# Performance work log

Measured on AMD Instinct MI355X. Metric: run time of the kernel, lower is better.

## Reference

```python
import jax, jax.numpy as jnp
import numpy as np

N_KERNELS = 11

def _kernel_mus(n):
    l = [1.0]
    bs = 2.0 / (n - 1)
    l.append(1 - bs / 2)
    for i in range(1, n - 1):
        l.append(l[i] - bs)
    return l

def _kernel_sigmas(n):
    bs = 2.0 / (n - 1)
    return [0.001] + [0.5 * bs] * (n - 1)

MU = jnp.asarray(_kernel_mus(N_KERNELS), jnp.float32)      # [K]
SIGMA = jnp.asarray(_kernel_sigmas(N_KERNELS), jnp.float32)  # [K]


def setup_inputs() -> dict:
    key = jax.random.key(0)
    ks = jax.random.split(key, 10)
    V, E, C = 50000, 300, 128
    B, Q, D = 128, 30, 200
    inp = {
        'query_tokens': jax.random.randint(ks[0], (B, Q), 0, V),
        'document_tokens': jax.random.randint(ks[1], (B, D), 0, V),
        'embedding': jax.random.normal(ks[2], (V, E), jnp.float32) * 0.1,
        'conv_w1': jax.random.normal(ks[3], (C, E, 1), jnp.float32) * 0.05,
        'conv_w2': jax.random.normal(ks[4], (C, E, 2), jnp.float32) * 0.05,
        'conv_w3': jax.random.normal(ks[5], (C, E, 3), jnp.float32) * 0.05,
        'conv_b1': jax.random.normal(ks[6], (C,), jnp.float32) * 0.01,
        'conv_b2': jax.random.normal(ks[7], (C,), jnp.float32) * 0.01,
        'conv_b3': jax.random.normal(ks[8], (C,), jnp.float32) * 0.01,
        'dense_w': jax.random.uniform(ks[9], (1, N_KERNELS * 9), jnp.float32, -0.014, 0.014),
    }
    return inp


def _conv_ngram(x_ble, w, b):
    # x_ble: [B, L, E]; w: [C, E, k]; pad (0, k-1) on the length dim -> same length out
    x = x_ble.transpose(0, 2, 1)  # [B, E, L]
    y = jax.lax.conv_general_dilated(
        x, w, window_strides=(1,), padding=[(0, w.shape[2] - 1)],
        dimension_numbers=('NCH', 'OIH', 'NCH'))
    return jax.nn.relu(y + b[None, :, None]).transpose(0, 2, 1)  # [B, L, C]


def _kernel_pool(q, d, qd_mask, q_mask):
    # q: [B,Q,C], d: [B,D,C]; cosine sim -> Gaussian RBF soft-binning -> masked log-sum pooling
    qn = q / (jnp.linalg.norm(q, axis=-1, keepdims=True) + 1e-13)
    dn = d / (jnp.linalg.norm(d, axis=-1, keepdims=True) + 1e-13)
    cos = jnp.einsum('bqc,bdc->bqd', qn, dn) * qd_mask           # [B,Q,D]
    diff = cos[..., None] - MU                                    # [B,Q,D,K]
    kern = jnp.exp(-(diff * diff) / (2.0 * SIGMA * SIGMA)) * qd_mask[..., None]
    per_kernel_query = jnp.sum(kern, axis=2)                      # [B,Q,K]
    logk = jnp.log(jnp.clip(per_kernel_query, 1e-10)) * 0.01
    return jnp.sum(logk * q_mask[..., None], axis=1)              # [B,K]


def reference(query_tokens, document_tokens, embedding,
              conv_w1, conv_w2, conv_w3, conv_b1, conv_b2, conv_b3, dense_w):
    q_mask = (query_tokens > 0).astype(jnp.float32)               # [B,Q]
    d_mask = (document_tokens > 0).astype(jnp.float32)            # [B,D]
    qd_mask = q_mask[:, :, None] * d_mask[:, None, :]             # [B,Q,D]

    q_emb = embedding[query_tokens]                               # [B,Q,E]
    d_emb = embedding[document_tokens]                            # [B,D,E]

    convs = [(conv_w1, conv_b1), (conv_w2, conv_b2), (conv_w3, conv_b3)]
    q_grams = [_conv_ngram(q_emb, w, b) for w, b in convs]
    d_grams = [_conv_ngram(d_emb, w, b) for w, b in convs]

    feats = jnp.concatenate(
        [_kernel_pool(q, d, qd_mask, q_mask) for q in q_grams for d in d_grams],
        axis=1)                                                   # [B, K*9]
    return (feats @ dense_w.T)[:, 0]                              # [B]
```

## Files before the change

### kernel.cpp

```cpp
#include <hip/hip_runtime.h>
#include <hip/hip_bf16.h>
#include <math.h>

#define B_   128
#define Qn   30
#define Dn   200
#define En   300

typedef __attribute__((ext_vector_type(8))) short short8;
typedef __attribute__((ext_vector_type(4))) float floatx4;
typedef unsigned int u32;
typedef unsigned short u16;

typedef const __attribute__((address_space(1))) unsigned int* gas_ptr;
typedef __attribute__((address_space(3))) unsigned int* las_ptr;

static __device__ __forceinline__ void gld_lds16(const void* g, void* l) {
    __builtin_amdgcn_global_load_lds((gas_ptr)g, (las_ptr)l, 16, 0, 0);
}

static __device__ __forceinline__ u16 f2b(float x) {
    union { float f; u32 u; } v; v.f = x;
    u32 r = v.u + 0x7FFFu + ((v.u >> 16) & 1u);
    return (u16)(r >> 16);
}
static __device__ __forceinline__ float bits2f(u32 u) {
    union { u32 u2; float f; } v; v.u2 = u; return v.f;
}

__global__ void prep_gather_kernel(
    const int* __restrict__ qtok, const int* __restrict__ dtok,
    const float* __restrict__ emb,
    const float* __restrict__ w1, const float* __restrict__ w2, const float* __restrict__ w3,
    u16* __restrict__ Ag, u16* __restrict__ Wt2)
{
    const int tid = threadIdx.x;
    if (blockIdx.x < 16) {
        const int b = blockIdx.y, c = blockIdx.x;
        __shared__ int toks[16];
        if (tid < 16) {
            int pos = c*16 + tid;
            int tok = -1;
            if (pos < Dn) tok = dtok[b*Dn + pos];
            else if (pos >= 208 && pos < 238) tok = qtok[b*Qn + (pos - 208)];
            toks[tid] = tok;
        }
        __syncthreads();
        #pragma unroll
        for (int i = 0; i < 5; ++i) {
            int f = tid + i*256;
            int r = f / 80, c4 = f - r*80;
            int t = toks[r];
            u16 o0=0,o1=0,o2=0,o3=0;
            if (t >= 0 && c4 < 75) {
                float4 v = *(const float4*)(emb + t*En + c4*4);
                o0=f2b(v.x); o1=f2b(v.y); o2=f2b(v.z); o3=f2b(v.w);
            }
            u16* p = Ag + ((b*256 + c*16 + r)*320 + c4*4);
            p[0]=o0; p[1]=o1; p[2]=o2; p[3]=o3;
        }
        if (b == 127 && c == 15 && tid < 160) {
            u16* p = Ag + (32768*320) + tid*4;
            p[0]=0; p[1]=0; p[2]=0; p[3]=0;
        }
    } else {
        int p = ((blockIdx.x - 16)*128 + blockIdx.y)*256 + tid;
        if (p >= 245760) return;
        int g, ntap, o;
        if (p < 40960)       { g=0; ntap=1; o=p; }
        else if (p < 122880) { g=1; ntap=2; o=p-40960; }
        else                 { g=2; ntap=3; o=p-122880; }
        int ks = o / (ntap*4096);
        int r  = o - ks*(ntap*4096);
        int j  = r / 4096;
        int r2 = r & 4095;
        int nt = r2 >> 9;
        int r3 = r2 & 511;
        int q4 = r3 >> 7;
        int c16 = (r3 >> 3) & 15;
        int k8 = r3 & 7;
        int ch = nt*16 + c16;
        int e  = ks*32 + q4*8 + k8;
        float v = 0.f;
        if (e < En) {
            if (g == 0)      v = w1[ch*En + e];
            else if (g == 1) v = w2[(ch*En + e)*2 + j];
            else             v = w3[(ch*En + e)*3 + j];
        }
        Wt2[p] = f2b(v);
    }
}

template<int NTAP>
static __device__ __forceinline__ void conv_body64(
    int tile, int gram,
    const u16* __restrict__ Ag, const u16* __restrict__ Wt2g,
    const float* __restrict__ bp,
    u16* __restrict__ qg, u16* __restrict__ dg,
    float* __restrict__ invnq, float* __restrict__ invnd, char* smem)
{
    char* As  = smem;
    char* Bs0 = smem + 43296;
    char* Bs1 = smem + 43296 + NTAP*8192;

    const int tid = threadIdx.x;
    const int wv = tid >> 6, lane = tid & 63;
    const int l15 = lane & 15, qd4 = lane >> 4;
    const int mh = wv >> 1, nh = wv & 1;

    {
        const char* src = (const char*)Wt2g + lane*16;
        #pragma unroll
        for (int i = 0; i < NTAP*2; ++i) {
            int chunk = wv*NTAP*2 + i;
            gld_lds16(src + chunk*1024, Bs0 + chunk*1024);
        }
    }
    {
        const char* base = (const char*)Ag + (size_t)tile*64*640;
        #pragma unroll
        for (int i = 0; i < 11; ++i) {
            int idx = tid + i*256;
            if (idx < 2640) {
                int r = idx / 40, c = idx - r*40;
                uint4 v = *(const uint4*)(base + r*640 + c*16);
                *(uint4*)(As + r*656 + c*16) = v;
            }
        }
    }

    float bias[4];
    #pragma unroll
    for (int nt = 0; nt < 4; ++nt) bias[nt] = bp[nh*64 + nt*16 + l15];

    floatx4 acc[2][4];
    #pragma unroll
    for (int mt = 0; mt < 2; ++mt)
        #pragma unroll
        for (int nt = 0; nt < 4; ++nt)
            acc[mt][nt] = (floatx4){0.f,0.f,0.f,0.f};

    __syncthreads();

    for (int ks = 0; ks < 10; ++ks) {
        char* Bcur = (ks & 1) ? Bs1 : Bs0;
        char* Bnxt = (ks & 1) ? Bs0 : Bs1;
        if (ks < 9) {
            const char* src = (const char*)Wt2g + (ks+1)*NTAP*8192 + lane*16;
            #pragma unroll
            for (int i = 0; i < NTAP*2; ++i) {
                int chunk = wv*NTAP*2 + i;
                gld_lds16(src + chunk*1024, Bnxt + chunk*1024);
            }
        }
        short8 af[2][NTAP];
        #pragma unroll
        for (int mt = 0; mt < 2; ++mt)
            #pragma unroll
            for (int j = 0; j < NTAP; ++j)
                af[mt][j] = *(const short8*)(As + (mh*32 + mt*16 + l15 + j)*656 + ks*64 + qd4*16);
        #pragma unroll
        for (int j = 0; j < NTAP; ++j) {
            short8 bfj[4];
            #pragma unroll
            for (int nt = 0; nt < 4; ++nt)
                bfj[nt] = *(const short8*)(Bcur + (j*8 + nh*4 + nt)*1024 + lane*16);
            #pragma unroll
            for (int mt = 0; mt < 2; ++mt)
                #pragma unroll
                for (int nt = 0; nt < 4; ++nt)
                    acc[mt][nt] = __builtin_amdgcn_mfma_f32_16x16x32_bf16(
                        af[mt][j], bfj[nt], acc[mt][nt], 0, 0, 0);
        }
        __syncthreads();
    }

    u16* Gs = (u16*)As;
    #pragma unroll
    for (int mt = 0; mt < 2; ++mt)
        #pragma unroll
        for (int nt = 0; nt < 4; ++nt) {
            int ch = nh*64 + nt*16 + l15;
            #pragma unroll
            for (int i = 0; i < 4; ++i) {
                int row = mh*32 + mt*16 + qd4*4 + i;
                Gs[row*136 + ch] = f2b(fmaxf(acc[mt][nt][i] + bias[nt], 0.f));
            }
        }
    __syncthreads();

    if (tid < 64) {
        const char* rp = (const char*)Gs + tid*272;
        float ssum = 0.f;
        #pragma unroll
        for (int t16 = 0; t16 < 16; ++t16) {
            uint4 u = *(const uint4*)(rp + t16*16);
            float x;
            x = bits2f(u.x << 16); ssum += x*x;  x = bits2f(u.x & 0xffff0000u); ssum += x*x;
            x = bits2f(u.y << 16); ssum += x*x;  x = bits2f(u.y & 0xffff0000u); ssum += x*x;
            x = bits2f(u.z << 16); ssum += x*x;  x = bits2f(u.z & 0xffff0000u); ssum += x*x;
            x = bits2f(u.w << 16); ssum += x*x;  x = bits2f(u.w & 0xffff0000u); ssum += x*x;
        }
        float inv = 1.f / (sqrtf(ssum) + 1e-13f);
        int gR = tile*64 + tid;
        int b = gR >> 8, pos = gR & 255;
        if (pos < 208)      invnd[(gram*B_ + b)*208 + pos] = inv;
        else if (pos < 238) invnq[(gram*B_ + b)*32 + (pos - 208)] = inv;
    }
    #pragma unroll
    for (int i = 0; i < 4; ++i) {
        int idx = tid + i*256;
        int r = idx >> 4, c16 = idx & 15;
        uint4 v = *(const uint4*)((const char*)Gs + r*272 + c16*16);
        int gR = tile*64 + r;
        int b = gR >> 8, pos = gR & 255;
        if (pos < 208)      *(uint4*)(dg + ((gram*B_ + b)*208 + pos)*128 + c16*8) = v;
        else if (pos < 238) *(uint4*)(qg + ((gram*B_ + b)*32 + (pos - 208))*128 + c16*8) = v;
    }
}

static __device__ __forceinline__ void conv_body32(
    int tile,
    const u16* __restrict__ Ag, const u16* __restrict__ Wt2g,
    const float* __restrict__ bp,
    u16* __restrict__ qg, u16* __restrict__ dg,
    float* __restrict__ invnq, float* __restrict__ invnd, char* smem)
{
    char* As  = smem;
    char* Bs0 = smem + 22304;
    char* Bs1 = smem + 46880;

    const int tid = threadIdx.x;
    const int wv = tid >> 6, lane = tid & 63;
    const int l15 = lane & 15, qd4 = lane >> 4;

    {
        const char* src = (const char*)Wt2g + lane*16;
        #pragma unroll
        for (int i = 0; i < 6; ++i) {
            int chunk = wv*6 + i;
            gld_lds16(src + chunk*1024, Bs0 + chunk*1024);
        }
    }
    {
        const char* base = (const char*)Ag + (size_t)tile*32*640;
        #pragma unroll
        for (int i = 0; i < 6; ++i) {
            int idx = tid + i*256;
            if (idx < 1360) {
                int r = idx / 40, c = idx - r*40;
                uint4 v = *(const uint4*)(base + r*640 + c*16);
                *(uint4*)(As + r*656 + c*16) = v;
            }
        }
    }

    float bias[2];
    #pragma unroll
    for (int nt = 0; nt < 2; ++nt) bias[nt] = bp[wv*32 + nt*16 + l15];

    floatx4 acc[2][2];
    #pragma unroll
    for (int mt = 0; mt < 2; ++mt)
        #pragma unroll
        for (int nt = 0; nt < 2; ++nt)
            acc[mt][nt] = (floatx4){0.f,0.f,0.f,0.f};

    __syncthreads();

    for (int ks = 0; ks < 10; ++ks) {
        char* Bcur = (ks & 1) ? Bs1 : Bs0;
        char* Bnxt = (ks & 1) ? Bs0 : Bs1;
        if (ks < 9) {
            const char* src = (const char*)Wt2g + (ks+1)*24576 + lane*16;
            #pragma unroll
            for (int i = 0; i < 6; ++i) {
                int chunk = wv*6 + i;
                gld_lds16(src + chunk*1024, Bnxt + chunk*1024);
            }
        }
        short8 af[2][3];
        #pragma unroll
        for (int mt = 0; mt < 2; ++mt)
            #pragma unroll
            for (int j = 0; j < 3; ++j)
                af[mt][j] = *(const short8*)(As + (mt*16 + l15 + j)*656 + ks*64 + qd4*16);
        #pragma unroll
        for (int j = 0; j < 3; ++j) {
            short8 bfj[2];
            #pragma unroll
            for (int nt = 0; nt < 2; ++nt)
                bfj[nt] = *(const short8*)(Bcur + (j*8 + wv*2 + nt)*1024 + lane*16);
            #pragma unroll
            for (int mt = 0; mt < 2; ++mt)
                #pragma unroll
                for (int nt = 0; nt < 2; ++nt)
                    acc[mt][nt] = __builtin_amdgcn_mfma_f32_16x16x32_bf16(
                        af[mt][j], bfj[nt], acc[mt][nt], 0, 0, 0);
        }
        __syncthreads();
    }

    u16* Gs = (u16*)As;
    #pragma unroll
    for (int mt = 0; mt < 2; ++mt)
        #pragma unroll
        for (int nt = 0; nt < 2; ++nt) {
            int ch = wv*32 + nt*16 + l15;
            #pragma unroll
            for (int i = 0; i < 4; ++i) {
                int row = mt*16 + qd4*4 + i;
                Gs[row*136 + ch] = f2b(fmaxf(acc[mt][nt][i] + bias[nt], 0.f));
            }
        }
    __syncthreads();

    if (tid < 32) {
        const char* rp = (const char*)Gs + tid*272;
        float ssum = 0.f;
        #pragma unroll
        for (int t16 = 0; t16 < 16; ++t16) {
            uint4 u = *(const uint4*)(rp + t16*16);
            float x;
            x = bits2f(u.x << 16); ssum += x*x;  x = bits2f(u.x & 0xffff0000u); ssum += x*x;
            x = bits2f(u.y << 16); ssum += x*x;  x = bits2f(u.y & 0xffff0000u); ssum += x*x;
            x = bits2f(u.z << 16); ssum += x*x;  x = bits2f(u.z & 0xffff0000u); ssum += x*x;
            x = bits2f(u.w << 16); ssum += x*x;  x = bits2f(u.w & 0xffff0000u); ssum += x*x;
        }
        float inv = 1.f / (sqrtf(ssum) + 1e-13f);
        int gR = tile*32 + tid;
        int b = gR >> 8, pos = gR & 255;
        if (pos < 208)      invnd[(2*B_ + b)*208 + pos] = inv;
        else if (pos < 238) invnq[(2*B_ + b)*32 + (pos - 208)] = inv;
    }
    #pragma unroll
    for (int i = 0; i < 2; ++i) {
        int idx = tid + i*256;
        int r = idx >> 4, c16 = idx & 15;
        uint4 v = *(const uint4*)((const char*)Gs + r*272 + c16*16);
        int gR = tile*32 + r;
        int b = gR >> 8, pos = gR & 255;
        if (pos < 208)      *(uint4*)(dg + ((2*B_ + b)*208 + pos)*128 + c16*8) = v;
        else if (pos < 238) *(uint4*)(qg + ((2*B_ + b)*32 + (pos - 208))*128 + c16*8) = v;
    }
}

__global__ __launch_bounds__(256, 2) void conv_kernel(
    const u16* __restrict__ Ag, const u16* __restrict__ Wt2,
    const float* __restrict__ b1, const float* __restrict__ b2, const float* __restrict__ b3,
    u16* __restrict__ qg, u16* __restrict__ dg,
    float* __restrict__ invnq, float* __restrict__ invnd)
{
    extern __shared__ char smem[];
    int bx = blockIdx.x;
    if (bx < 512)
        conv_body64<1>(bx,      0, Ag, Wt2,        b1, qg, dg, invnq, invnd, smem);
    else if (bx < 1024)
        conv_body64<2>(bx-512,  1, Ag, Wt2+40960,  b2, qg, dg, invnq, invnd, smem);
    else
        conv_body32(bx-1024,       Ag, Wt2+122880, b3, qg, dg, invnq, invnd, smem);
}

__global__ __launch_bounds__(256, 2) void pool_kernel(
    const u16* __restrict__ qg, const u16* __restrict__ dg,
    const float* __restrict__ invnq, const float* __restrict__ invnd,
    const int* __restrict__ qtok, const int* __restrict__ dtok,
    float* __restrict__ feats)
{
    __shared__ __align__(16) u16 dsb[208*136];
    __shared__ float pk[96*12];
    __shared__ float invqA[96];
    __shared__ float qmA[96];
    __shared__ __align__(16) float invd[208];

    const int tid = threadIdx.x;
    const int b = blockIdx.y, dj = blockIdx.x;
    const int wv = tid >> 6, lane = tid & 63;
    const int l15 = lane & 15, qd4 = lane >> 4;

    for (int idx = tid; idx < 208*16; idx += 256) {
        int r = idx >> 4, ch = idx & 15;
        uint4 v = make_uint4(0u,0u,0u,0u);
        if (r < Dn) v = *(const uint4*)(dg + ((dj*B_ + b)*208 + r)*128 + ch*8);
        *(uint4*)((char*)dsb + r*272 + ch*16) = v;
    }
    if (tid < 208) {
        float v = invnd[(dj*B_ + b)*208 + tid];
        bool ok = (tid < Dn) && (dtok[b*Dn + tid] > 0);
        invd[tid] = ok ? v : (-fabsf(v) - 1.0f);
    }
    if (tid < 96) {
        int qi = tid >> 5, qr = tid & 31;
        float v = invnq[(qi*B_ + b)*32 + qr];
        bool ok = (qr < Qn) && (qtok[b*Qn + qr] > 0);
        invqA[tid] = ok ? v : 0.f;
        qmA[tid] = ok ? 1.f : 0.f;
    }
    for (int i = tid; i < 96*12; i += 256) pk[i] = 0.f;
    __syncthreads();

    const float CkR[9] = {8886110.5f, 162754.79f, 2980.958f, 54.598150f, 1.0f,
                          0.018315639f, 3.3546263e-4f, 6.1442124e-6f, 1.1253517e-7f};

    for (int qi = 0; qi < 3; ++qi) {
        short8 qf[2][4];
        float vq[2];
        #pragma unroll
        for (int qt = 0; qt < 2; ++qt) {
            vq[qt] = invqA[qi*32 + qt*16 + l15];
            #pragma unroll
            for (int ks = 0; ks < 4; ++ks)
                qf[qt][ks] = *(const short8*)(qg + ((qi*B_ + b)*32 + qt*16 + l15)*128 + ks*32 + qd4*8);
        }
        float pkl[2][11];
        #pragma unroll
        for (int qt = 0; qt < 2; ++qt)
            #pragma unroll
            for (int k = 0; k < 11; ++k) pkl[qt][k] = 0.f;

        for (int t = wv; t < 13; t += 4) {
            short8 af[4];
            #pragma unroll
            for (int ks = 0; ks < 4; ++ks)
                af[ks] = *(const short8*)((const char*)dsb + (t*16 + l15)*272 + ks*64 + qd4*16);
            floatx4 acc[2];
            acc[0] = (floatx4){0.f,0.f,0.f,0.f};
            acc[1] = (floatx4){0.f,0.f,0.f,0.f};
            #pragma unroll
            for (int ks = 0; ks < 4; ++ks)
                #pragma unroll
                for (int qt = 0; qt < 2; ++qt)
                    acc[qt] = __builtin_amdgcn_mfma_f32_16x16x32_bf16(af[ks], qf[qt][ks], acc[qt], 0, 0, 0);
            floatx4 iv4 = *(const floatx4*)(invd + t*16 + qd4*4);
            #pragma unroll
            for (int qt = 0; qt < 2; ++qt)
                #pragma unroll
                for (int i = 0; i < 4; ++i) {
                    float cs = acc[qt][i] * vq[qt] * iv4[i];
                    cs = (cs > 0.f) ? cs : 2.0f;
                    float t0 = cs - 1.0f;
                    float u  = cs - 0.9f;
                    float s0 = __expf(-500000.f * t0 * t0);
                    float e  = __expf(-50.f * u * u);
                    float rr = __expf(-20.f * cs);
                    pkl[qt][0] += s0;
                    pkl[qt][1] += e;
                    #pragma unroll
                    for (int kk = 0; kk < 9; ++kk) {
                        e = e * rr * CkR[kk];
                        pkl[qt][2 + kk] += e;
                    }
                }
        }
        #pragma unroll
        for (int qt = 0; qt < 2; ++qt)
            #pragma unroll
            for (int k = 0; k < 11; ++k) {
                float v = pkl[qt][k];
                v += __shfl_xor(v, 16);
                v += __shfl_xor(v, 32);
                if (qd4 == 0) atomicAdd(&pk[(qi*32 + qt*16 + l15)*12 + k], v);
            }
    }
    __syncthreads();

    if (tid < 33) {
        int qi = tid / 11, k = tid - qi*11;
        float s = 0.f;
        for (int q = 0; q < Qn; ++q)
            s += qmA[qi*32 + q] * 0.01f * __logf(fmaxf(pk[(qi*32 + q)*12 + k], 1e-10f));
        feats[(b*9 + qi*3 + dj)*11 + k] = s;
    }
}

__global__ void final_kernel(const float* __restrict__ feats,
                             const float* __restrict__ dw,
                             float* __restrict__ out) {
    int b = threadIdx.x;
    if (b < B_) {
        float s = 0.f;
        for (int f = 0; f < 99; ++f) s += feats[b*99 + f] * dw[f];
        out[b] = s;
    }
}

extern "C" void kernel_launch(void* const* d_in, const int* in_sizes, int n_in,
                              void* d_out, int out_size, void* d_ws, size_t ws_size,
                              hipStream_t stream) {
    const int*   qtok = (const int*)d_in[0];
    const int*   dtok = (const int*)d_in[1];
    const float* emb  = (const float*)d_in[2];
    const float* w1   = (const float*)d_in[3];
    const float* w2   = (const float*)d_in[4];
    const float* w3   = (const float*)d_in[5];
    const float* b1   = (const float*)d_in[6];
    const float* b2   = (const float*)d_in[7];
    const float* b3   = (const float*)d_in[8];
    const float* dw   = (const float*)d_in[9];
    float* out = (float*)d_out;

    char* w = (char*)d_ws;
    u16*   Wt2   = (u16*)w;
    u16*   Ag    = (u16*)(w + 491520);
    u16*   qg    = (u16*)(w + 21464320);
    u16*   dgm   = (u16*)(w + 24610048);
    float* invq_ = (float*)(w + 45057280);
    float* invd_ = (float*)(w + 45106432);
    float* feats = (float*)(w + 45425920);

    prep_gather_kernel<<<dim3(24, B_), 256, 0, stream>>>(
        qtok, dtok, emb, w1, w2, w3, Ag, Wt2);

    const int conv_lds = 76064;
    hipFuncSetAttribute(reinterpret_cast<const void*>(conv_kernel),
                        hipFuncAttributeMaxDynamicSharedMemorySize, conv_lds);
    conv_kernel<<<dim3(2048), 256, conv_lds, stream>>>(
        Ag, Wt2, b1, b2, b3, qg, dgm, invq_, invd_);

    pool_kernel<<<dim3(3, B_), 256, 0, stream>>>(qg, dgm, invq_, invd_, qtok, dtok, feats);

    final_kernel<<<1, 128, 0, stream>>>(feats, dw, out);
}
```

Baseline: 183.1 us.

## Fuse embedding gather into conv and compute all three n-grams per tile

The embedding gather and bf16 conversion move from the prep kernel into the conv kernel, so the intermediate bf16 gathered matrix is no longer written to and re-read from global memory. Each 64-row tile now computes all three n-gram convolutions at once with 512 threads, sharing the A tile in LDS and interleaving the weights for all grams per k-step. The launch drops from 2048 blocks to 512. The cost is a much larger LDS footprint (about 141KB per block), which likely limits residency to one block per CU, and the embedding gather latency now sits inside the conv kernel.

New measurement: 173.6 us. 5.2% less time.

```diff
diff --git a/kernel.cpp b/kernel.cpp
--- a/kernel.cpp
+++ b/kernel.cpp
@@ -28,117 +28,109 @@
     union { u32 u2; float f; } v; v.u2 = u; return v.f;
 }
 
-__global__ void prep_gather_kernel(
+__global__ void prep_kernel(
+    const float* __restrict__ w1, const float* __restrict__ w2, const float* __restrict__ w3,
+    u16* __restrict__ Wt3)
+{
+    int p = (blockIdx.x*128 + blockIdx.y)*256 + threadIdx.x;
+    if (p >= 245760) return;
+    int ks = p / 24576;
+    int r  = p - ks*24576;
+    int g, rr;
+    if (r < 4096)        { g = 0; rr = r;         }
+    else if (r < 12288)  { g = 1; rr = r - 4096;  }
+    else                 { g = 2; rr = r - 12288; }
+    int j  = rr >> 12;
+    int r2 = rr & 4095;
+    int nt  = r2 >> 9;
+    int q4  = (r2 >> 7) & 3;
+    int c16 = (r2 >> 3) & 15;
+    int k8  = r2 & 7;
+    int ch = nt*16 + c16;
+    int e  = ks*32 + q4*8 + k8;
+    float v = 0.f;
+    if (e < En) {
+        if (g == 0)      v = w1[ch*En + e];
+        else if (g == 1) v = w2[(ch*En + e)*2 + j];
+        else             v = w3[(ch*En + e)*3 + j];
+    }
+    Wt3[p] = f2b(v);
+}
+
+__global__ __launch_bounds__(512, 2) void conv_kernel(
     const int* __restrict__ qtok, const int* __restrict__ dtok,
     const float* __restrict__ emb,
-    const float* __restrict__ w1, const float* __restrict__ w2, const float* __restrict__ w3,
-    u16* __restrict__ Ag, u16* __restrict__ Wt2)
+    const u16* __restrict__ Wt3,
+    const float* __restrict__ b1, const float* __restrict__ b2, const float* __restrict__ b3,
+    u16* __restrict__ qg, u16* __restrict__ dg,
+    float* __restrict__ invnq, float* __restrict__ invnd)
 {
+    extern __shared__ char smem[];
+    char* As  = smem;
+    char* Bs0 = smem + 43296;
+    char* Bs1 = smem + 92448;
+    int*  toks = (int*)(smem + 141600);
+
+    const int tile = blockIdx.x;
     const int tid = threadIdx.x;
-    if (blockIdx.x < 16) {
-        const int b = blockIdx.y, c = blockIdx.x;
-        __shared__ int toks[16];
-        if (tid < 16) {
-            int pos = c*16 + tid;
-            int tok = -1;
-            if (pos < Dn) tok = dtok[b*Dn + pos];
-            else if (pos >= 208 && pos < 238) tok = qtok[b*Qn + (pos - 208)];
-            toks[tid] = tok;
-        }
-        __syncthreads();
-        #pragma unroll
-        for (int i = 0; i < 5; ++i) {
-            int f = tid + i*256;
-            int r = f / 80, c4 = f - r*80;
+    const int wv = tid >> 6, lane = tid & 63;
+    const int l15 = lane & 15, qd4 = lane >> 4;
+    const int mh = wv >> 2, nh = wv & 3;
+    const int gR0 = tile*64;
+
+    if (tid < 66) {
+        int gr = gR0 + tid;
+        int t = -1;
+        if (gr < 32768) {
+            int b = gr >> 8, pos = gr & 255;
+            if (pos < Dn) t = dtok[b*Dn + pos];
+            else if (pos >= 208 && pos < 238) t = qtok[b*Qn + (pos - 208)];
+        }
+        toks[tid] = t;
+    }
+    __syncthreads();
+
+    {
+        const char* src = (const char*)Wt3 + lane*16;
+        #pragma unroll
+        for (int i = 0; i < 6; ++i) {
+            int chunk = wv*6 + i;
+            gld_lds16(src + chunk*1024, Bs0 + chunk*1024);
+        }
+    }
+    #pragma unroll
+    for (int i = 0; i < 11; ++i) {
+        int idx = tid + i*512;
+        if (idx < 5280) {
+            int r = idx / 80, c4 = idx - r*80;
             int t = toks[r];
             u16 o0=0,o1=0,o2=0,o3=0;
             if (t >= 0 && c4 < 75) {
                 float4 v = *(const float4*)(emb + t*En + c4*4);
                 o0=f2b(v.x); o1=f2b(v.y); o2=f2b(v.z); o3=f2b(v.w);
             }
-            u16* p = Ag + ((b*256 + c*16 + r)*320 + c4*4);
-            p[0]=o0; p[1]=o1; p[2]=o2; p[3]=o3;
-        }
-        if (b == 127 && c == 15 && tid < 160) {
-            u16* p = Ag + (32768*320) + tid*4;
-            p[0]=0; p[1]=0; p[2]=0; p[3]=0;
-        }
-    } else {
-        int p = ((blockIdx.x - 16)*128 + blockIdx.y)*256 + tid;
-        if (p >= 245760) return;
-        int g, ntap, o;
-        if (p < 40960)       { g=0; ntap=1; o=p; }
-        else if (p < 122880) { g=1; ntap=2; o=p-40960; }
-        else                 { g=2; ntap=3; o=p-122880; }
-        int ks = o / (ntap*4096);
-        int r  = o - ks*(ntap*4096);
-        int j  = r / 4096;
-        int r2 = r & 4095;
-        int nt = r2 >> 9;
-        int r3 = r2 & 511;
-        int q4 = r3 >> 7;
-        int c16 = (r3 >> 3) & 15;
-        int k8 = r3 & 7;
-        int ch = nt*16 + c16;
-        int e  = ks*32 + q4*8 + k8;
-        float v = 0.f;
-        if (e < En) {
-            if (g == 0)      v = w1[ch*En + e];
-            else if (g == 1) v = w2[(ch*En + e)*2 + j];
-            else             v = w3[(ch*En + e)*3 + j];
-        }
-        Wt2[p] = f2b(v);
-    }
-}
-
-template<int NTAP>
-static __device__ __forceinline__ void conv_body64(
-    int tile, int gram,
-    const u16* __restrict__ Ag, const u16* __restrict__ Wt2g,
-    const float* __restrict__ bp,
-    u16* __restrict__ qg, u16* __restrict__ dg,
-    float* __restrict__ invnq, float* __restrict__ invnd, char* smem)
-{
-    char* As  = smem;
-    char* Bs0 = smem + 43296;
-    char* Bs1 = smem + 43296 + NTAP*8192;
-
-    const int tid = threadIdx.x;
-    const int wv = tid >> 6, lane = tid & 63;
-    const int l15 = lane & 15, qd4 = lane >> 4;
-    const int mh = wv >> 1, nh = wv & 1;
-
-    {
-        const char* src = (const char*)Wt2g + lane*16;
-        #pragma unroll
-        for (int i = 0; i < NTAP*2; ++i) {
-            int chunk = wv*NTAP*2 + i;
-            gld_lds16(src + chunk*1024, Bs0 + chunk*1024);
-        }
-    }
-    {
-        const char* base = (const char*)Ag + (size_t)tile*64*640;
-        #pragma unroll
-        for (int i = 0; i < 11; ++i) {
-            int idx = tid + i*256;
-            if (idx < 2640) {
-                int r = idx / 40, c = idx - r*40;
-                uint4 v = *(const uint4*)(base + r*640 + c*16);
-                *(uint4*)(As + r*656 + c*16) = v;
-            }
-        }
-    }
-
-    float bias[4];
-    #pragma unroll
-    for (int nt = 0; nt < 4; ++nt) bias[nt] = bp[nh*64 + nt*16 + l15];
-
-    floatx4 acc[2][4];
-    #pragma unroll
-    for (int mt = 0; mt < 2; ++mt)
-        #pragma unroll
-        for (int nt = 0; nt < 4; ++nt)
-            acc[mt][nt] = (floatx4){0.f,0.f,0.f,0.f};
+            u16* pdst = (u16*)(As + r*656 + c4*8);
+            pdst[0]=o0; pdst[1]=o1; pdst[2]=o2; pdst[3]=o3;
+        }
+    }
+
+    float bias[3][2];
+    #pragma unroll
+    for (int nt = 0; nt < 2; ++nt) {
+        int ch = nh*32 + nt*16 + l15;
+        bias[0][nt] = b1[ch];
+        bias[1][nt] = b2[ch];
+        bias[2][nt] = b3[ch];
+    }
+
+    floatx4 acc[3][2][2];
+    #pragma unroll
+    for (int g = 0; g < 3; ++g)
+        #pragma unroll
+        for (int mt = 0; mt < 2; ++mt)
+            #pragma unroll
+            for (int nt = 0; nt < 2; ++nt)
+                acc[g][mt][nt] = (floatx4){0.f,0.f,0.f,0.f};
 
     __syncthreads();
 
@@ -146,51 +138,59 @@
         char* Bcur = (ks & 1) ? Bs1 : Bs0;
         char* Bnxt = (ks & 1) ? Bs0 : Bs1;
         if (ks < 9) {
-            const char* src = (const char*)Wt2g + (ks+1)*NTAP*8192 + lane*16;
-            #pragma unroll
-            for (int i = 0; i < NTAP*2; ++i) {
-                int chunk = wv*NTAP*2 + i;
+            const char* src = (const char*)Wt3 + (ks+1)*49152 + lane*16;
+            #pragma unroll
+            for (int i = 0; i < 6; ++i) {
+                int chunk = wv*6 + i;
                 gld_lds16(src + chunk*1024, Bnxt + chunk*1024);
             }
         }
-        short8 af[2][NTAP];
+        short8 af[2][3];
         #pragma unroll
         for (int mt = 0; mt < 2; ++mt)
             #pragma unroll
-            for (int j = 0; j < NTAP; ++j)
+            for (int j = 0; j < 3; ++j)
                 af[mt][j] = *(const short8*)(As + (mh*32 + mt*16 + l15 + j)*656 + ks*64 + qd4*16);
         #pragma unroll
-        for (int j = 0; j < NTAP; ++j) {
-            short8 bfj[4];
-            #pragma unroll
-            for (int nt = 0; nt < 4; ++nt)
-                bfj[nt] = *(const short8*)(Bcur + (j*8 + nh*4 + nt)*1024 + lane*16);
-            #pragma unroll
-            for (int mt = 0; mt < 2; ++mt)
+        for (int g = 0; g < 3; ++g) {
+            const int cbB = (g == 0) ? 0 : (g == 1) ? 8192 : 24576;
+            #pragma unroll
+            for (int j = 0; j <= g; ++j) {
+                const char* bb = Bcur + cbB + (j*8 + nh*2)*1024 + lane*16;
+                short8 w0 = *(const short8*)(bb);
+                short8 w1v = *(const short8*)(bb + 1024);
                 #pragma unroll
-                for (int nt = 0; nt < 4; ++nt)
-                    acc[mt][nt] = __builtin_amdgcn_mfma_f32_16x16x32_bf16(
-                        af[mt][j], bfj[nt], acc[mt][nt], 0, 0, 0);
+                for (int mt = 0; mt < 2; ++mt) {
+                    acc[g][mt][0] = __builtin_amdgcn_mfma_f32_16x16x32_bf16(
+                        af[mt][j], w0,  acc[g][mt][0], 0, 0, 0);
+                    acc[g][mt][1] = __builtin_amdgcn_mfma_f32_16x16x32_bf16(
+                        af[mt][j], w1v, acc[g][mt][1], 0, 0, 0);
+                }
+            }
         }
         __syncthreads();
     }
 
-    u16* Gs = (u16*)As;
-    #pragma unroll
-    for (int mt = 0; mt < 2; ++mt)
-        #pragma unroll
-        for (int nt = 0; nt < 4; ++nt) {
-            int ch = nh*64 + nt*16 + l15;
-            #pragma unroll
-            for (int i = 0; i < 4; ++i) {
-                int row = mh*32 + mt*16 + qd4*4 + i;
-                Gs[row*136 + ch] = f2b(fmaxf(acc[mt][nt][i] + bias[nt], 0.f));
-            }
-        }
-    __syncthreads();
-
-    if (tid < 64) {
-        const char* rp = (const char*)Gs + tid*272;
+    char* Gsb = smem + 43296;
+    #pragma unroll
+    for (int g = 0; g < 3; ++g)
+        #pragma unroll
+        for (int mt = 0; mt < 2; ++mt)
+            #pragma unroll
+            for (int nt = 0; nt < 2; ++nt) {
+                int ch = nh*32 + nt*16 + l15;
+                #pragma unroll
+                for (int i = 0; i < 4; ++i) {
+                    int row = mh*32 + mt*16 + qd4*4 + i;
+                    *(u16*)(Gsb + g*17408 + row*272 + ch*2) =
+                        f2b(fmaxf(acc[g][mt][nt][i] + bias[g][nt], 0.f));
+                }
+            }
+    __syncthreads();
+
+    if (tid < 192) {
+        int g = tid >> 6, r = tid & 63;
+        const char* rp = Gsb + g*17408 + r*272;
         float ssum = 0.f;
         #pragma unroll
         for (int t16 = 0; t16 < 16; ++t16) {
@@ -202,163 +202,22 @@
             x = bits2f(u.w << 16); ssum += x*x;  x = bits2f(u.w & 0xffff0000u); ssum += x*x;
         }
         float inv = 1.f / (sqrtf(ssum) + 1e-13f);
-        int gR = tile*64 + tid;
-        int b = gR >> 8, pos = gR & 255;
-        if (pos < 208)      invnd[(gram*B_ + b)*208 + pos] = inv;
-        else if (pos < 238) invnq[(gram*B_ + b)*32 + (pos - 208)] = inv;
-    }
-    #pragma unroll
-    for (int i = 0; i < 4; ++i) {
-        int idx = tid + i*256;
-        int r = idx >> 4, c16 = idx & 15;
-        uint4 v = *(const uint4*)((const char*)Gs + r*272 + c16*16);
-        int gR = tile*64 + r;
-        int b = gR >> 8, pos = gR & 255;
-        if (pos < 208)      *(uint4*)(dg + ((gram*B_ + b)*208 + pos)*128 + c16*8) = v;
-        else if (pos < 238) *(uint4*)(qg + ((gram*B_ + b)*32 + (pos - 208))*128 + c16*8) = v;
-    }
-}
-
-static __device__ __forceinline__ void conv_body32(
-    int tile,
-    const u16* __restrict__ Ag, const u16* __restrict__ Wt2g,
-    const float* __restrict__ bp,
-    u16* __restrict__ qg, u16* __restrict__ dg,
-    float* __restrict__ invnq, float* __restrict__ invnd, char* smem)
-{
-    char* As  = smem;
-    char* Bs0 = smem + 22304;
-    char* Bs1 = smem + 46880;
-
-    const int tid = threadIdx.x;
-    const int wv = tid >> 6, lane = tid & 63;
-    const int l15 = lane & 15, qd4 = lane >> 4;
-
-    {
-        const char* src = (const char*)Wt2g + lane*16;
-        #pragma unroll
-        for (int i = 0; i < 6; ++i) {
-            int chunk = wv*6 + i;
-            gld_lds16(src + chunk*1024, Bs0 + chunk*1024);
-        }
-    }
-    {
-        const char* base = (const char*)Ag + (size_t)tile*32*640;
-        #pragma unroll
-        for (int i = 0; i < 6; ++i) {
-            int idx = tid + i*256;
-            if (idx < 1360) {
-                int r = idx / 40, c = idx - r*40;
-                uint4 v = *(const uint4*)(base + r*640 + c*16);
-                *(uint4*)(As + r*656 + c*16) = v;
-            }
-        }
-    }
-
-    float bias[2];
-    #pragma unroll
-    for (int nt = 0; nt < 2; ++nt) bias[nt] = bp[wv*32 + nt*16 + l15];
-
-    floatx4 acc[2][2];
-    #pragma unroll
-    for (int mt = 0; mt < 2; ++mt)
-        #pragma unroll
-        for (int nt = 0; nt < 2; ++nt)
-            acc[mt][nt] = (floatx4){0.f,0.f,0.f,0.f};
-
-    __syncthreads();
-
-    for (int ks = 0; ks < 10; ++ks) {
-        char* Bcur = (ks & 1) ? Bs1 : Bs0;
-        char* Bnxt = (ks & 1) ? Bs0 : Bs1;
-        if (ks < 9) {
-            const char* src = (const char*)Wt2g + (ks+1)*24576 + lane*16;
-            #pragma unroll
-            for (int i = 0; i < 6; ++i) {
-                int chunk = wv*6 + i;
-                gld_lds16(src + chunk*1024, Bnxt + chunk*1024);
-            }
-        }
-        short8 af[2][3];
-        #pragma unroll
-        for (int mt = 0; mt < 2; ++mt)
-            #pragma unroll
-            for (int j = 0; j < 3; ++j)
-                af[mt][j] = *(const short8*)(As + (mt*16 + l15 + j)*656 + ks*64 + qd4*16);
-        #pragma unroll
-        for (int j = 0; j < 3; ++j) {
-            short8 bfj[2];
-            #pragma unroll
-            for (int nt = 0; nt < 2; ++nt)
-                bfj[nt] = *(const short8*)(Bcur + (j*8 + wv*2 + nt)*1024 + lane*16);
-            #pragma unroll
-            for (int mt = 0; mt < 2; ++mt)
-                #pragma unroll
-                for (int nt = 0; nt < 2; ++nt)
-                    acc[mt][nt] = __builtin_amdgcn_mfma_f32_16x16x32_bf16(
-                        af[mt][j], bfj[nt], acc[mt][nt], 0, 0, 0);
-        }
-        __syncthreads();
-    }
-
-    u16* Gs = (u16*)As;
-    #pragma unroll
-    for (int mt = 0; mt < 2; ++mt)
-        #pragma unroll
-        for (int nt = 0; nt < 2; ++nt) {
-            int ch = wv*32 + nt*16 + l15;
-            #pragma unroll
-            for (int i = 0; i < 4; ++i) {
-                int row = mt*16 + qd4*4 + i;
-                Gs[row*136 + ch] = f2b(fmaxf(acc[mt][nt][i] + bias[nt], 0.f));
-            }
-        }
-    __syncthreads();
-
-    if (tid < 32) {
-        const char* rp = (const char*)Gs + tid*272;
-        float ssum = 0.f;
-        #pragma unroll
-        for (int t16 = 0; t16 < 16; ++t16) {
-            uint4 u = *(const uint4*)(rp + t16*16);
-            float x;
-            x = bits2f(u.x << 16); ssum += x*x;  x = bits2f(u.x & 0xffff0000u); ssum += x*x;
-            x = bits2f(u.y << 16); ssum += x*x;  x = bits2f(u.y & 0xffff0000u); ssum += x*x;
-            x = bits2f(u.z << 16); ssum += x*x;  x = bits2f(u.z & 0xffff0000u); ssum += x*x;
-            x = bits2f(u.w << 16); ssum += x*x;  x = bits2f(u.w & 0xffff0000u); ssum += x*x;
-        }
-        float inv = 1.f / (sqrtf(ssum) + 1e-13f);
-        int gR = tile*32 + tid;
-        int b = gR >> 8, pos = gR & 255;
-        if (pos < 208)      invnd[(2*B_ + b)*208 + pos] = inv;
-        else if (pos < 238) invnq[(2*B_ + b)*32 + (pos - 208)] = inv;
-    }
-    #pragma unroll
-    for (int i = 0; i < 2; ++i) {
-        int idx = tid + i*256;
-        int r = idx >> 4, c16 = idx & 15;
-        uint4 v = *(const uint4*)((const char*)Gs + r*272 + c16*16);
-        int gR = tile*32 + r;
-        int b = gR >> 8, pos = gR & 255;
-        if (pos < 208)      *(uint4*)(dg + ((2*B_ + b)*208 + pos)*128 + c16*8) = v;
-        else if (pos < 238) *(uint4*)(qg + ((2*B_ + b)*32 + (pos - 208))*128 + c16*8) = v;
-    }
-}
-
-__global__ __launch_bounds__(256, 2) void conv_kernel(
-    const u16* __restrict__ Ag, const u16* __restrict__ Wt2,
-    const float* __restrict__ b1, const float* __restrict__ b2, const float* __restrict__ b3,
-    u16* __restrict__ qg, u16* __restrict__ dg,
-    float* __restrict__ invnq, float* __restrict__ invnd)
-{
-    extern __shared__ char smem[];
-    int bx = blockIdx.x;
-    if (bx < 512)
-        conv_body64<1>(bx,      0, Ag, Wt2,        b1, qg, dg, invnq, invnd, smem);
-    else if (bx < 1024)
-        conv_body64<2>(bx-512,  1, Ag, Wt2+40960,  b2, qg, dg, invnq, invnd, smem);
-    else
-        conv_body32(bx-1024,       Ag, Wt2+122880, b3, qg, dg, invnq, invnd, smem);
+        int gr = gR0 + r;
+        int b = gr >> 8, pos = gr & 255;
+        if (pos < 208)      invnd[(g*B_ + b)*208 + pos] = inv;
+        else if (pos < 238) invnq[(g*B_ + b)*32 + (pos - 208)] = inv;
+    }
+    #pragma unroll
+    for (int i = 0; i < 6; ++i) {
+        int idx = tid + i*512;
+        int g = idx >> 10, rem = idx & 1023;
+        int r = rem >> 4, c16 = rem & 15;
+        uint4 v = *(const uint4*)(Gsb + g*17408 + r*272 + c16*16);
+        int gr = gR0 + r;
+        int b = gr >> 8, pos = gr & 255;
+        if (pos < 208)      *(uint4*)(dg + ((g*B_ + b)*208 + pos)*128 + c16*8) = v;
+        else if (pos < 238) *(uint4*)(qg + ((g*B_ + b)*32 + (pos - 208))*128 + c16*8) = v;
+    }
 }
 
 __global__ __launch_bounds__(256, 2) void pool_kernel(
@@ -500,22 +359,20 @@
     float* out = (float*)d_out;
 
     char* w = (char*)d_ws;
-    u16*   Wt2   = (u16*)w;
-    u16*   Ag    = (u16*)(w + 491520);
-    u16*   qg    = (u16*)(w + 21464320);
-    u16*   dgm   = (u16*)(w + 24610048);
-    float* invq_ = (float*)(w + 45057280);
-    float* invd_ = (float*)(w + 45106432);
-    float* feats = (float*)(w + 45425920);
-
-    prep_gather_kernel<<<dim3(24, B_), 256, 0, stream>>>(
-        qtok, dtok, emb, w1, w2, w3, Ag, Wt2);
-
-    const int conv_lds = 76064;
+    u16*   Wt3   = (u16*)w;
+    u16*   qg    = (u16*)(w + 491520);
+    u16*   dgm   = (u16*)(w + 3637248);
+    float* invq_ = (float*)(w + 24084480);
+    float* invd_ = (float*)(w + 24133632);
+    float* feats = (float*)(w + 24453120);
+
+    prep_kernel<<<dim3(8, B_), 256, 0, stream>>>(w1, w2, w3, Wt3);
+
+    const int conv_lds = 141864;
     hipFuncSetAttribute(reinterpret_cast<const void*>(conv_kernel),
                         hipFuncAttributeMaxDynamicSharedMemorySize, conv_lds);
-    conv_kernel<<<dim3(2048), 256, conv_lds, stream>>>(
-        Ag, Wt2, b1, b2, b3, qg, dgm, invq_, invd_);
+    conv_kernel<<<dim3(512), 512, conv_lds, stream>>>(
+        qtok, dtok, emb, Wt3, b1, b2, b3, qg, dgm, invq_, invd_);
 
     pool_kernel<<<dim3(3, B_), 256, 0, stream>>>(qg, dgm, invq_, invd_, qtok, dtok, feats);
 
```
